# Performance work log

Measured on AMD Instinct MI355X. Metric: run time of the kernel, lower is better.

Reference implementation:

```python
import jax, jax.numpy as jnp
import numpy as np

EPS = 1e-12

def l2_normalize(x, axis=-1):
    # matches torch F.normalize(p=2, dim=1, eps=1e-12) for 2D input
    n = jnp.sqrt(jnp.sum(x * x, axis=axis, keepdims=True))
    return x / jnp.maximum(n, EPS)

def setup_inputs() -> dict:
    key = jax.random.key(0)
    ks = jax.random.split(key, 7)
    N, D = 8192, 256
    s = 1.0 / np.sqrt(D)
    x = jax.random.normal(ks[0], (N, D), dtype=jnp.float32)
    Wq = jax.random.uniform(ks[1], (D, D), jnp.float32, -s, s)
    bq = jax.random.uniform(ks[2], (D,), jnp.float32, -s, s)
    Wk = jax.random.uniform(ks[3], (D, D), jnp.float32, -s, s)
    bk = jax.random.uniform(ks[4], (D,), jnp.float32, -s, s)
    Wv = jax.random.uniform(ks[5], (D, D), jnp.float32, -s, s)
    bv = jax.random.uniform(ks[6], (D,), jnp.float32, -s, s)
    return {"x": x, "Wq": Wq, "bq": bq, "Wk": Wk, "bk": bk, "Wv": Wv, "bv": bv}

def reference(x, Wq, bq, Wk, bk, Wv, bv):
    q = l2_normalize(x @ Wq.T + bq)           # [N, D]
    k = l2_normalize(x @ Wk.T + bk)           # [N, D]
    v = x @ Wv.T + bv                         # [N, D]
    cos_sim = q @ k.T                         # [N, N]
    w = jax.nn.relu(cos_sim)
    # zero diagonal, then renormalize rows to sum 1
    N = w.shape[0]
    w = jnp.where(jnp.eye(N, dtype=bool), 0.0, w)
    w = w / jnp.maximum(jnp.sum(w, axis=-1, keepdims=True), EPS)
    return w @ v + x
```

## Files before the change

### kernel.cpp

```cpp
#include <hip/hip_runtime.h>

#define NROWS 8192
#define DDIM  256
#define KSPLIT 4
#define BM 128
#define BK 64
#define NT (NROWS / KSPLIT / BK)

typedef __bf16 bf16x8 __attribute__((ext_vector_type(8)));
typedef float  f32x4  __attribute__((ext_vector_type(4)));
typedef float  f32x16 __attribute__((ext_vector_type(16)));

typedef __attribute__((address_space(1))) unsigned int uint_gas;
typedef __attribute__((address_space(3))) unsigned int uint_las;

__device__ __forceinline__ void gload_lds16(const void* g, void* l) {
  __builtin_amdgcn_global_load_lds((const uint_gas*)g, (uint_las*)l, 16, 0, 0);
}

__device__ __forceinline__ unsigned int f2bf_bits(float f) {
  union { float f; unsigned int u; } v; v.f = f;
  unsigned int r = v.u + 0x7FFFu + ((v.u >> 16) & 1u);
  return r >> 16;
}
__device__ __forceinline__ float bf2f(unsigned int b) {
  union { unsigned int u; float f; } v; v.u = b << 16;
  return v.f;
}
__device__ __forceinline__ unsigned int pack2bf(float a, float b) {
  union { unsigned int u; __bf16 h[2]; } p;
  p.h[0] = (__bf16)a; p.h[1] = (__bf16)b;
  return p.u;
}
__device__ __forceinline__ unsigned short f2h_bits(float f) {
  union { _Float16 h; unsigned short u; } c; c.h = (_Float16)f;
  return c.u;
}
__device__ __forceinline__ float h2f(unsigned short u) {
  union { unsigned short u; _Float16 h; } c; c.u = u;
  return (float)c.h;
}

__global__ __launch_bounds__(256) void convert_kernel(
    const float* __restrict__ x, const float* __restrict__ wq,
    const float* __restrict__ wk, const float* __restrict__ wv,
    unsigned short* __restrict__ xb, unsigned short* __restrict__ Wb)
{
  int i = blockIdx.x * 256 + threadIdx.x;
  const int nx4 = NROWS * DDIM / 4;
  const int nw4 = DDIM * DDIM / 4;
  const float4* src; unsigned short* dst; int j;
  if (i < nx4)              { src = (const float4*)x;  dst = xb;                j = i; }
  else if (i < nx4 +   nw4) { src = (const float4*)wq; dst = Wb;                j = i - nx4; }
  else if (i < nx4 + 2*nw4) { src = (const float4*)wk; dst = Wb + DDIM*DDIM;    j = i - nx4 - nw4; }
  else                      { src = (const float4*)wv; dst = Wb + 2*DDIM*DDIM;  j = i - nx4 - 2*nw4; }
  float4 f = src[j];
  ushort4 o;
  o.x = (unsigned short)f2bf_bits(f.x);
  o.y = (unsigned short)f2bf_bits(f.y);
  o.z = (unsigned short)f2bf_bits(f.z);
  o.w = (unsigned short)f2bf_bits(f.w);
  ((ushort4*)dst)[j] = o;
}

__global__ __launch_bounds__(256) void qkv_kernel(
    const float* __restrict__ bq, const float* __restrict__ bk, const float* __restrict__ bv,
    const unsigned short* __restrict__ xb, const unsigned short* __restrict__ Wb,
    unsigned short* __restrict__ qb, unsigned short* __restrict__ kb,
    unsigned short* __restrict__ vb, unsigned short* __restrict__ vT)
{
  __shared__ unsigned short vstage[DDIM * 72];
  const int t = threadIdx.x;
  const int w = t >> 6, l = t & 63;
  const int c = l & 15, g = l >> 4;
  const int out = blockIdx.x / 128;
  const int mb  = blockIdx.x % 128;
  const int row0 = mb * 64;
  const int rw = row0 + w * 16;

  bf16x8 a[8];
  #pragma unroll
  for (int ks = 0; ks < 8; ks++)
    a[ks] = *(const bf16x8*)(xb + (size_t)(rw + c) * DDIM + ks * 32 + g * 8);

  const unsigned short* W = Wb + out * DDIM * DDIM;
  const float* bias = (out == 0) ? bq : (out == 1) ? bk : bv;
  unsigned short* dst = (out == 0) ? qb : (out == 1) ? kb : vb;
  f32x4 vals[16];
  #pragma unroll
  for (int ct = 0; ct < 16; ct++) {
    f32x4 acc = {0.f, 0.f, 0.f, 0.f};
    #pragma unroll
    for (int ks = 0; ks < 8; ks++) {
      bf16x8 b = *(const bf16x8*)(W + (size_t)(ct * 16 + c) * DDIM + ks * 32 + g * 8);
      acc = __builtin_amdgcn_mfma_f32_16x16x32_bf16(a[ks], b, acc, 0, 0, 0);
    }
    float bias_v = bias[ct * 16 + c];
    #pragma unroll
    for (int r = 0; r < 4; r++) acc[r] += bias_v;
    vals[ct] = acc;
  }
  if (out < 2) {
    #pragma unroll
    for (int r = 0; r < 4; r++) {
      float ss = 0.f;
      #pragma unroll
      for (int ct = 0; ct < 16; ct++) ss += vals[ct][r] * vals[ct][r];
      ss += __shfl_xor(ss, 1); ss += __shfl_xor(ss, 2);
      ss += __shfl_xor(ss, 4); ss += __shfl_xor(ss, 8);
      float inv = 1.f / fmaxf(sqrtf(ss), 1e-12f);
      #pragma unroll
      for (int ct = 0; ct < 16; ct++) vals[ct][r] *= inv;
    }
  }
  #pragma unroll
  for (int ct = 0; ct < 16; ct++) {
    #pragma unroll
    for (int r = 0; r < 4; r++) {
      unsigned int bits = f2bf_bits(vals[ct][r]);
      unsigned int ob = (unsigned int)__shfl_xor((int)bits, 1);
      if (!(l & 1))
        *(unsigned int*)(dst + (size_t)(rw + g * 4 + r) * DDIM + ct * 16 + c) =
            bits | (ob << 16);
      if (out == 2)
        vstage[(ct * 16 + c) * 72 + (w * 16 + g * 4 + r)] = (unsigned short)bits;
    }
  }
  if (out == 2) {
    __syncthreads();
    #pragma unroll
    for (int p = 0; p < 8; p++) {
      int dd = (t >> 3) + p * 32;
      int ch = t & 7;
      *(uint4*)(vT + (size_t)dd * NROWS + row0 + ch * 8) =
          *(const uint4*)(vstage + dd * 72 + ch * 8);
    }
  }
}

__global__ __launch_bounds__(512, 2) void attn_kernel(
    const unsigned short* __restrict__ qb, const unsigned short* __restrict__ kb,
    const unsigned short* __restrict__ vT,
    unsigned short* __restrict__ nump, float* __restrict__ denp)
{
  __shared__ __align__(16) char smem[163840];
  char* kbuf = smem;
  char* vbuf = smem + 65536;
  char* Pb   = smem + 131072;

  const int t = threadIdx.x;
  const int w = t >> 6, l = t & 63;
  const int l31 = l & 31, hi = l >> 5;
  const int sr = w >> 1, sc = w & 1;
  const int pr = w >> 2, pc = w & 3;
  const int bid = blockIdx.x;
  const int split = bid & (KSPLIT - 1);
  const int mb = bid >> 2;
  const int q0 = mb * BM;
  const int kbase0 = split * (NROWS / KSPLIT);

  const char* kbc = (const char*)kb;
  const char* vtc = (const char*)vT;

  bf16x8 qa[16];
  {
    const unsigned short* qrowp = qb + (size_t)(q0 + sr * 32 + l31) * DDIM + hi * 8;
    #pragma unroll
    for (int m = 0; m < 16; m++)
      qa[m] = *(const bf16x8*)(qrowp + m * 16);
  }

  f32x16 oacc[2][2];
  #pragma unroll
  for (int rt = 0; rt < 2; rt++)
    #pragma unroll
    for (int dt = 0; dt < 2; dt++)
      oacc[rt][dt] = (f32x16){0.f};
  float denl = 0.f;

  auto stageK = [&](int buf, int it) {
    const int kbase = kbase0 + it * BK;
    const char* ksrc = kbc + (size_t)kbase * 512;
    #pragma unroll
    for (int i = 0; i < 4; i++) {
      int n = i * 512 + t;
      int row = n >> 5, slot = n & 31;
      gload_lds16(ksrc + row * 512 + (((slot - row) & 31) << 4),
                  kbuf + buf * 32768 + i * 8192 + w * 1024);
    }
  };
  auto stageV = [&](int buf, int it) {
    const int kbase = kbase0 + it * BK;
    const char* vsrc = vtc + (size_t)kbase * 2;
    #pragma unroll
    for (int i = 0; i < 4; i++) {
      int n = i * 512 + t;
      int dd = n >> 3, slot = n & 7;
      gload_lds16(vsrc + (size_t)dd * (NROWS * 2) + ((slot ^ (dd & 7)) * 16),
                  vbuf + buf * 32768 + i * 8192 + w * 1024);
    }
  };

  stageK(0, 0);
  asm volatile("s_waitcnt vmcnt(0)" ::: "memory");
  __builtin_amdgcn_sched_barrier(0);
  __builtin_amdgcn_s_barrier();
  __builtin_amdgcn_sched_barrier(0);

  const int qrow = sr * 32 + l31;
  char* prowP = (char*)0;
  const int pswz = (qrow & 7) << 4;
  const int krl = sc * 32 + l31;

  for (int it = 0; it < NT; ++it) {
    const int cur = it & 1;
    if (it + 1 < NT) stageK(cur ^ 1, it + 1);
    stageV(cur, it);
    __builtin_amdgcn_sched_barrier(0);

    const char* kcur = kbuf + cur * 32768;
    f32x16 sacc = (f32x16){0.f};
    #pragma unroll
    for (int m = 0; m < 16; m++) {
      bf16x8 kf = *(const bf16x8*)(kcur + krl * 512 +
                                   (((m * 2 + hi + krl) & 31) << 4));
      sacc = __builtin_amdgcn_mfma_f32_32x32x16_bf16(kf, qa[m], sacc, 0, 0, 0);
    }
    prowP = Pb + cur * 16384 + qrow * 128;
    #pragma unroll
    for (int q = 0; q < 4; q++) {
      float v0 = fmaxf(sacc[4 * q + 0], 0.f);
      float v1 = fmaxf(sacc[4 * q + 1], 0.f);
      float v2 = fmaxf(sacc[4 * q + 2], 0.f);
      float v3 = fmaxf(sacc[4 * q + 3], 0.f);
      denl += (v0 + v1) + (v2 + v3);
      uint2 d2;
      d2.x = pack2bf(v0, v1);
      d2.y = pack2bf(v2, v3);
      *(uint2*)(prowP + ((sc * 64 + q * 16 + hi * 8) ^ pswz)) = d2;
    }

    if (it > 0) {
      const char* Pprev = Pb + (cur ^ 1) * 16384;
      const char* vcur  = vbuf + (cur ^ 1) * 32768;
      const int pr0 = pr * 64 + l31;
      const int pr1 = pr * 64 + 32 + l31;
      #pragma unroll
      for (int ch = 0; ch < 4; ch++) {
        const int cb = ch * 32 + hi * 16;
        bf16x8 pa0 = *(const bf16x8*)(Pprev + pr0 * 128 + (cb ^ ((pr0 & 7) << 4)));
        bf16x8 pa1 = *(const bf16x8*)(Pprev + pr1 * 128 + (cb ^ ((pr1 & 7) << 4)));
        #pragma unroll
        for (int dt = 0; dt < 2; dt++) {
          int dl = pc * 64 + dt * 32 + l31;
          bf16x8 vf = *(const bf16x8*)(vcur + dl * 128 + (cb ^ ((dl & 7) << 4)));
          oacc[0][dt] = __builtin_amdgcn_mfma_f32_32x32x16_bf16(pa0, vf, oacc[0][dt], 0, 0, 0);
          oacc[1][dt] = __builtin_amdgcn_mfma_f32_32x32x16_bf16(pa1, vf, oacc[1][dt], 0, 0, 0);
        }
      }
    }
    asm volatile("s_waitcnt lgkmcnt(0)" ::: "memory");
    __builtin_amdgcn_sched_barrier(0);
    asm volatile("s_waitcnt vmcnt(0)" ::: "memory");
    __builtin_amdgcn_sched_barrier(0);
    __builtin_amdgcn_s_barrier();
    __builtin_amdgcn_sched_barrier(0);
  }

  {
    const int last = (NT - 1) & 1;
    const char* Pprev = Pb + last * 16384;
    const char* vcur  = vbuf + last * 32768;
    const int pr0 = pr * 64 + l31;
    const int pr1 = pr * 64 + 32 + l31;
    #pragma unroll
    for (int ch = 0; ch < 4; ch++) {
      const int cb = ch * 32 + hi * 16;
      bf16x8 pa0 = *(const bf16x8*)(Pprev + pr0 * 128 + (cb ^ ((pr0 & 7) << 4)));
      bf16x8 pa1 = *(const bf16x8*)(Pprev + pr1 * 128 + (cb ^ ((pr1 & 7) << 4)));
      #pragma unroll
      for (int dt = 0; dt < 2; dt++) {
        int dl = pc * 64 + dt * 32 + l31;
        bf16x8 vf = *(const bf16x8*)(vcur + dl * 128 + (cb ^ ((dl & 7) << 4)));
        oacc[0][dt] = __builtin_amdgcn_mfma_f32_32x32x16_bf16(pa0, vf, oacc[0][dt], 0, 0, 0);
        oacc[1][dt] = __builtin_amdgcn_mfma_f32_32x32x16_bf16(pa1, vf, oacc[1][dt], 0, 0, 0);
      }
    }
  }

  unsigned short* np = nump + (size_t)split * NROWS * DDIM;
  #pragma unroll
  for (int rt = 0; rt < 2; rt++)
    #pragma unroll
    for (int dt = 0; dt < 2; dt++)
      #pragma unroll
      for (int r = 0; r < 16; r++) {
        int rowg = q0 + pr * 64 + rt * 32 + (r & 3) + 8 * (r >> 2) + 4 * hi;
        int col  = pc * 64 + dt * 32 + l31;
        np[(size_t)rowg * DDIM + col] = f2h_bits(oacc[rt][dt][r]);
      }
  {
    float d = denl;
    d += __shfl_xor(d, 32);
    if (l < 32)
      denp[((size_t)split * 2 + sc) * NROWS + q0 + sr * 32 + l] = d;
  }
}

__global__ __launch_bounds__(256) void combine_kernel(
    const float* __restrict__ x, const unsigned short* __restrict__ qb,
    const unsigned short* __restrict__ kb, const unsigned short* __restrict__ vb,
    const unsigned short* __restrict__ nump, const float* __restrict__ denp,
    float* __restrict__ out)
{
  const int t = threadIdx.x;
  const int w = t >> 6, l = t & 63;
  const int i = blockIdx.x * 4 + w;

  ushort4 q4 = *(const ushort4*)(qb + (size_t)i * DDIM + l * 4);
  ushort4 k4 = *(const ushort4*)(kb + (size_t)i * DDIM + l * 4);
  float s = bf2f(q4.x) * bf2f(k4.x) + bf2f(q4.y) * bf2f(k4.y)
          + bf2f(q4.z) * bf2f(k4.z) + bf2f(q4.w) * bf2f(k4.w);
  #pragma unroll
  for (int m = 1; m < 64; m <<= 1) s += __shfl_xor(s, m);
  float r  = fmaxf(s, 0.f);
  float rb = bf2f(f2bf_bits(r));

  float den = 0.f;
  #pragma unroll
  for (int sp = 0; sp < KSPLIT * 2; sp++)
    den += denp[(size_t)sp * NROWS + i];
  float inv = 1.f / fmaxf(den - rb, 1e-12f);

  const int d0 = l * 4;
  float4 acc = {0.f, 0.f, 0.f, 0.f};
  #pragma unroll
  for (int sp = 0; sp < KSPLIT; sp++) {
    ushort4 u4 = *(const ushort4*)(nump + ((size_t)sp * NROWS + i) * DDIM + d0);
    acc.x += h2f(u4.x); acc.y += h2f(u4.y);
    acc.z += h2f(u4.z); acc.w += h2f(u4.w);
  }
  ushort4 v4 = *(const ushort4*)(vb + (size_t)i * DDIM + d0);
  float4 xx = *(const float4*)(x + (size_t)i * DDIM + d0);
  float4 o;
  o.x = (acc.x - rb * bf2f(v4.x)) * inv + xx.x;
  o.y = (acc.y - rb * bf2f(v4.y)) * inv + xx.y;
  o.z = (acc.z - rb * bf2f(v4.z)) * inv + xx.z;
  o.w = (acc.w - rb * bf2f(v4.w)) * inv + xx.w;
  *(float4*)(out + (size_t)i * DDIM + d0) = o;
}

extern "C" void kernel_launch(void* const* d_in, const int* in_sizes, int n_in,
                              void* d_out, int out_size, void* d_ws, size_t ws_size,
                              hipStream_t stream)
{
  const float* x  = (const float*)d_in[0];
  const float* Wq = (const float*)d_in[1];
  const float* bq = (const float*)d_in[2];
  const float* Wk = (const float*)d_in[3];
  const float* bk = (const float*)d_in[4];
  const float* Wv = (const float*)d_in[5];
  const float* bv = (const float*)d_in[6];

  char* ws = (char*)d_ws;
  unsigned short* xb   = (unsigned short*)(ws + 0);
  unsigned short* Wb   = (unsigned short*)(ws + 4194304);
  unsigned short* qb   = (unsigned short*)(ws + 4587520);
  unsigned short* kb   = (unsigned short*)(ws + 8781824);
  unsigned short* vb   = (unsigned short*)(ws + 12976128);
  unsigned short* vT   = (unsigned short*)(ws + 17170432);
  unsigned short* nump = (unsigned short*)(ws + 21364736);
  float* denp = (float*)(ws + 38141952);

  convert_kernel<<<2240, 256, 0, stream>>>(x, Wq, Wk, Wv, xb, Wb);
  qkv_kernel<<<384, 256, 0, stream>>>(bq, bk, bv, xb, Wb, qb, kb, vb, vT);
  attn_kernel<<<(NROWS / BM) * KSPLIT, 512, 0, stream>>>(qb, kb, vT, nump, denp);
  combine_kernel<<<NROWS / 4, 256, 0, stream>>>(x, qb, kb, vb, nump, denp, (float*)d_out);
}
```

Measured before the change: 126.2 us.

## Warp-specialize attention kernel into separate QK and PV wave groups

```diff
diff --git a/kernel.cpp b/kernel.cpp
--- a/kernel.cpp
+++ b/kernel.cpp
@@ -138,7 +138,7 @@
   }
 }
 
-__global__ __launch_bounds__(512, 2) void attn_kernel(
+__global__ __launch_bounds__(1024, 4) void attn_kernel(
     const unsigned short* __restrict__ qb, const unsigned short* __restrict__ kb,
     const unsigned short* __restrict__ vT,
     unsigned short* __restrict__ nump, float* __restrict__ denp)
@@ -151,100 +151,140 @@
   const int t = threadIdx.x;
   const int w = t >> 6, l = t & 63;
   const int l31 = l & 31, hi = l >> 5;
-  const int sr = w >> 1, sc = w & 1;
-  const int pr = w >> 2, pc = w & 3;
+  const int rw = w & 7;
+  const int ts = t & 511;
   const int bid = blockIdx.x;
   const int split = bid & (KSPLIT - 1);
   const int mb = bid >> 2;
   const int q0 = mb * BM;
   const int kbase0 = split * (NROWS / KSPLIT);
-
   const char* kbc = (const char*)kb;
   const char* vtc = (const char*)vT;
 
-  bf16x8 qa[16];
-  {
-    const unsigned short* qrowp = qb + (size_t)(q0 + sr * 32 + l31) * DDIM + hi * 8;
-    #pragma unroll
-    for (int m = 0; m < 16; m++)
-      qa[m] = *(const bf16x8*)(qrowp + m * 16);
-  }
-
-  f32x16 oacc[2][2];
-  #pragma unroll
-  for (int rt = 0; rt < 2; rt++)
-    #pragma unroll
-    for (int dt = 0; dt < 2; dt++)
-      oacc[rt][dt] = (f32x16){0.f};
-  float denl = 0.f;
-
-  auto stageK = [&](int buf, int it) {
-    const int kbase = kbase0 + it * BK;
-    const char* ksrc = kbc + (size_t)kbase * 512;
-    #pragma unroll
-    for (int i = 0; i < 4; i++) {
-      int n = i * 512 + t;
-      int row = n >> 5, slot = n & 31;
-      gload_lds16(ksrc + row * 512 + (((slot - row) & 31) << 4),
-                  kbuf + buf * 32768 + i * 8192 + w * 1024);
-    }
-  };
-  auto stageV = [&](int buf, int it) {
-    const int kbase = kbase0 + it * BK;
-    const char* vsrc = vtc + (size_t)kbase * 2;
-    #pragma unroll
-    for (int i = 0; i < 4; i++) {
-      int n = i * 512 + t;
-      int dd = n >> 3, slot = n & 7;
-      gload_lds16(vsrc + (size_t)dd * (NROWS * 2) + ((slot ^ (dd & 7)) * 16),
-                  vbuf + buf * 32768 + i * 8192 + w * 1024);
-    }
-  };
-
-  stageK(0, 0);
-  asm volatile("s_waitcnt vmcnt(0)" ::: "memory");
-  __builtin_amdgcn_sched_barrier(0);
-  __builtin_amdgcn_s_barrier();
-  __builtin_amdgcn_sched_barrier(0);
-
-  const int qrow = sr * 32 + l31;
-  char* prowP = (char*)0;
-  const int pswz = (qrow & 7) << 4;
-  const int krl = sc * 32 + l31;
-
-  for (int it = 0; it < NT; ++it) {
-    const int cur = it & 1;
-    if (it + 1 < NT) stageK(cur ^ 1, it + 1);
-    stageV(cur, it);
+  if (w < 8) {
+    const int sr = rw >> 1, sc = rw & 1;
+    const int qrow = sr * 32 + l31;
+    const int krl = sc * 32 + l31;
+    const int pswz = (qrow & 7) << 4;
+
+    bf16x8 qa[16];
+    {
+      const unsigned short* qrowp = qb + (size_t)(q0 + qrow) * DDIM + hi * 8;
+      #pragma unroll
+      for (int m = 0; m < 16; m++) qa[m] = *(const bf16x8*)(qrowp + m * 16);
+    }
+    float denl = 0.f;
+
+    auto stageK = [&](int buf, int it) {
+      const char* ksrc = kbc + (size_t)(kbase0 + it * BK) * 512;
+      #pragma unroll
+      for (int i = 0; i < 4; i++) {
+        int n = i * 512 + ts;
+        int row = n >> 5, slot = n & 31;
+        gload_lds16(ksrc + row * 512 + (((slot - row) & 31) << 4),
+                    kbuf + buf * 32768 + i * 8192 + rw * 1024);
+      }
+    };
+
+    stageK(0, 0);
+    asm volatile("s_waitcnt vmcnt(0)" ::: "memory");
     __builtin_amdgcn_sched_barrier(0);
-
-    const char* kcur = kbuf + cur * 32768;
-    f32x16 sacc = (f32x16){0.f};
-    #pragma unroll
-    for (int m = 0; m < 16; m++) {
-      bf16x8 kf = *(const bf16x8*)(kcur + krl * 512 +
-                                   (((m * 2 + hi + krl) & 31) << 4));
-      sacc = __builtin_amdgcn_mfma_f32_32x32x16_bf16(kf, qa[m], sacc, 0, 0, 0);
-    }
-    prowP = Pb + cur * 16384 + qrow * 128;
-    #pragma unroll
-    for (int q = 0; q < 4; q++) {
-      float v0 = fmaxf(sacc[4 * q + 0], 0.f);
-      float v1 = fmaxf(sacc[4 * q + 1], 0.f);
-      float v2 = fmaxf(sacc[4 * q + 2], 0.f);
-      float v3 = fmaxf(sacc[4 * q + 3], 0.f);
-      denl += (v0 + v1) + (v2 + v3);
-      uint2 d2;
-      d2.x = pack2bf(v0, v1);
-      d2.y = pack2bf(v2, v3);
-      *(uint2*)(prowP + ((sc * 64 + q * 16 + hi * 8) ^ pswz)) = d2;
-    }
-
-    if (it > 0) {
-      const char* Pprev = Pb + (cur ^ 1) * 16384;
-      const char* vcur  = vbuf + (cur ^ 1) * 32768;
-      const int pr0 = pr * 64 + l31;
-      const int pr1 = pr * 64 + 32 + l31;
+    __builtin_amdgcn_s_barrier();
+    __builtin_amdgcn_sched_barrier(0);
+
+    for (int it = 0; it < NT; ++it) {
+      const int cur = it & 1;
+      if (it + 1 < NT) stageK(cur ^ 1, it + 1);
+      __builtin_amdgcn_sched_barrier(0);
+
+      const char* kcur = kbuf + cur * 32768;
+      f32x16 sacc = (f32x16){0.f};
+      #pragma unroll
+      for (int m = 0; m < 16; m++) {
+        bf16x8 kf = *(const bf16x8*)(kcur + krl * 512 +
+                                     (((m * 2 + hi + krl) & 31) << 4));
+        sacc = __builtin_amdgcn_mfma_f32_32x32x16_bf16(kf, qa[m], sacc, 0, 0, 0);
+      }
+      char* prowP = Pb + cur * 16384 + qrow * 128;
+      #pragma unroll
+      for (int q = 0; q < 4; q++) {
+        float v0 = fmaxf(sacc[4 * q + 0], 0.f);
+        float v1 = fmaxf(sacc[4 * q + 1], 0.f);
+        float v2 = fmaxf(sacc[4 * q + 2], 0.f);
+        float v3 = fmaxf(sacc[4 * q + 3], 0.f);
+        denl += (v0 + v1) + (v2 + v3);
+        uint2 d2;
+        d2.x = pack2bf(v0, v1);
+        d2.y = pack2bf(v2, v3);
+        *(uint2*)(prowP + ((sc * 64 + q * 16 + hi * 8) ^ pswz)) = d2;
+      }
+      asm volatile("s_waitcnt vmcnt(0) lgkmcnt(0)" ::: "memory");
+      __builtin_amdgcn_sched_barrier(0);
+      __builtin_amdgcn_s_barrier();
+      __builtin_amdgcn_sched_barrier(0);
+    }
+
+    float d = denl;
+    d += __shfl_xor(d, 32);
+    if (l < 32)
+      denp[((size_t)split * 2 + sc) * NROWS + q0 + sr * 32 + l] = d;
+  } else {
+    const int pr = rw >> 2, pc = rw & 3;
+    const int pr0 = pr * 64 + l31, pr1 = pr * 64 + 32 + l31;
+
+    f32x16 oacc[2][2];
+    #pragma unroll
+    for (int rt = 0; rt < 2; rt++)
+      #pragma unroll
+      for (int dt = 0; dt < 2; dt++)
+        oacc[rt][dt] = (f32x16){0.f};
+
+    auto stageV = [&](int buf, int it) {
+      const char* vsrc = vtc + (size_t)(kbase0 + it * BK) * 2;
+      #pragma unroll
+      for (int i = 0; i < 4; i++) {
+        int n = i * 512 + ts;
+        int dd = n >> 3, slot = n & 7;
+        gload_lds16(vsrc + (size_t)dd * (NROWS * 2) + ((slot ^ (dd & 7)) * 16),
+                    vbuf + buf * 32768 + i * 8192 + rw * 1024);
+      }
+    };
+
+    __builtin_amdgcn_s_barrier();
+    __builtin_amdgcn_sched_barrier(0);
+
+    for (int it = 0; it < NT; ++it) {
+      const int cur = it & 1;
+      stageV(cur, it);
+      __builtin_amdgcn_sched_barrier(0);
+
+      if (it > 0) {
+        const char* Pprev = Pb + (cur ^ 1) * 16384;
+        const char* vprev = vbuf + (cur ^ 1) * 32768;
+        #pragma unroll
+        for (int ch = 0; ch < 4; ch++) {
+          const int cb = ch * 32 + hi * 16;
+          bf16x8 pa0 = *(const bf16x8*)(Pprev + pr0 * 128 + (cb ^ ((pr0 & 7) << 4)));
+          bf16x8 pa1 = *(const bf16x8*)(Pprev + pr1 * 128 + (cb ^ ((pr1 & 7) << 4)));
+          #pragma unroll
+          for (int dt = 0; dt < 2; dt++) {
+            int dl = pc * 64 + dt * 32 + l31;
+            bf16x8 vf = *(const bf16x8*)(vprev + dl * 128 + (cb ^ ((dl & 7) << 4)));
+            oacc[0][dt] = __builtin_amdgcn_mfma_f32_32x32x16_bf16(pa0, vf, oacc[0][dt], 0, 0, 0);
+            oacc[1][dt] = __builtin_amdgcn_mfma_f32_32x32x16_bf16(pa1, vf, oacc[1][dt], 0, 0, 0);
+          }
+        }
+      }
+      asm volatile("s_waitcnt vmcnt(0) lgkmcnt(0)" ::: "memory");
+      __builtin_amdgcn_sched_barrier(0);
+      __builtin_amdgcn_s_barrier();
+      __builtin_amdgcn_sched_barrier(0);
+    }
+
+    {
+      const int last = (NT - 1) & 1;
+      const char* Pprev = Pb + last * 16384;
+      const char* vprev = vbuf + last * 32768;
       #pragma unroll
       for (int ch = 0; ch < 4; ch++) {
         const int cb = ch * 32 + hi * 16;
@@ -253,57 +293,24 @@
         #pragma unroll
         for (int dt = 0; dt < 2; dt++) {
           int dl = pc * 64 + dt * 32 + l31;
-          bf16x8 vf = *(const bf16x8*)(vcur + dl * 128 + (cb ^ ((dl & 7) << 4)));
+          bf16x8 vf = *(const bf16x8*)(vprev + dl * 128 + (cb ^ ((dl & 7) << 4)));
           oacc[0][dt] = __builtin_amdgcn_mfma_f32_32x32x16_bf16(pa0, vf, oacc[0][dt], 0, 0, 0);
           oacc[1][dt] = __builtin_amdgcn_mfma_f32_32x32x16_bf16(pa1, vf, oacc[1][dt], 0, 0, 0);
         }
       }
     }
-    asm volatile("s_waitcnt lgkmcnt(0)" ::: "memory");
-    __builtin_amdgcn_sched_barrier(0);
-    asm volatile("s_waitcnt vmcnt(0)" ::: "memory");
-    __builtin_amdgcn_sched_barrier(0);
-    __builtin_amdgcn_s_barrier();
-    __builtin_amdgcn_sched_barrier(0);
-  }
-
-  {
-    const int last = (NT - 1) & 1;
-    const char* Pprev = Pb + last * 16384;
-    const char* vcur  = vbuf + last * 32768;
-    const int pr0 = pr * 64 + l31;
-    const int pr1 = pr * 64 + 32 + l31;
-    #pragma unroll
-    for (int ch = 0; ch < 4; ch++) {
-      const int cb = ch * 32 + hi * 16;
-      bf16x8 pa0 = *(const bf16x8*)(Pprev + pr0 * 128 + (cb ^ ((pr0 & 7) << 4)));
-      bf16x8 pa1 = *(const bf16x8*)(Pprev + pr1 * 128 + (cb ^ ((pr1 & 7) << 4)));
-      #pragma unroll
-      for (int dt = 0; dt < 2; dt++) {
-        int dl = pc * 64 + dt * 32 + l31;
-        bf16x8 vf = *(const bf16x8*)(vcur + dl * 128 + (cb ^ ((dl & 7) << 4)));
-        oacc[0][dt] = __builtin_amdgcn_mfma_f32_32x32x16_bf16(pa0, vf, oacc[0][dt], 0, 0, 0);
-        oacc[1][dt] = __builtin_amdgcn_mfma_f32_32x32x16_bf16(pa1, vf, oacc[1][dt], 0, 0, 0);
-      }
-    }
-  }
-
-  unsigned short* np = nump + (size_t)split * NROWS * DDIM;
-  #pragma unroll
-  for (int rt = 0; rt < 2; rt++)
-    #pragma unroll
-    for (int dt = 0; dt < 2; dt++)
-      #pragma unroll
-      for (int r = 0; r < 16; r++) {
-        int rowg = q0 + pr * 64 + rt * 32 + (r & 3) + 8 * (r >> 2) + 4 * hi;
-        int col  = pc * 64 + dt * 32 + l31;
-        np[(size_t)rowg * DDIM + col] = f2h_bits(oacc[rt][dt][r]);
-      }
-  {
-    float d = denl;
-    d += __shfl_xor(d, 32);
-    if (l < 32)
-      denp[((size_t)split * 2 + sc) * NROWS + q0 + sr * 32 + l] = d;
+
+    unsigned short* np = nump + (size_t)split * NROWS * DDIM;
+    #pragma unroll
+    for (int rt = 0; rt < 2; rt++)
+      #pragma unroll
+      for (int dt = 0; dt < 2; dt++)
+        #pragma unroll
+        for (int r = 0; r < 16; r++) {
+          int rowg = q0 + pr * 64 + rt * 32 + (r & 3) + 8 * (r >> 2) + 4 * hi;
+          int col  = pc * 64 + dt * 32 + l31;
+          np[(size_t)rowg * DDIM + col] = f2h_bits(oacc[rt][dt][r]);
+        }
   }
 }
 
@@ -374,6 +381,6 @@
 
   convert_kernel<<<2240, 256, 0, stream>>>(x, Wq, Wk, Wv, xb, Wb);
   qkv_kernel<<<384, 256, 0, stream>>>(bq, bk, bv, xb, Wb, qb, kb, vb, vT);
-  attn_kernel<<<(NROWS / BM) * KSPLIT, 512, 0, stream>>>(qb, kb, vT, nump, denp);
+  attn_kernel<<<(NROWS / BM) * KSPLIT, 1024, 0, stream>>>(qb, kb, vT, nump, denp);
   combine_kernel<<<NROWS / 4, 256, 0, stream>>>(x, qb, kb, vb, nump, denp, (float*)d_out);
 }
```

New measurement: 126.0 us. About the same (-0.2%).
